# Optimization experiments

Hardware: AMD Instinct MI355X
Metric: run time of the kernel (lower is better)

## Reference

```python
import jax, jax.numpy as jnp
import numpy as np

T, B, D, H = 512, 256, 256, 256


def setup_inputs() -> dict:
    key = jax.random.key(0)
    ks = jax.random.split(key, 10)
    # ragged lengths in [T//2, T], sorted descending as pack_padded_sequence requires
    lengths = np.sort(np.random.RandomState(0).randint(T // 2, T + 1, size=B))[::-1]
    # batch_sizes[t] = number of sequences still active at step t (non-increasing, >=1)
    batch_sizes = (lengths[None, :] > np.arange(T)[:, None]).sum(axis=1).astype(np.int32)
    batch_sizes = np.maximum(batch_sizes, 1)
    return {
        "input_x": jax.random.normal(ks[0], (T, B, D), jnp.float32),
        "h0": jax.random.normal(ks[1], (B, H), jnp.float32),
        "c0": jax.random.normal(ks[2], (B, H), jnp.float32),
        # variational dropout masks (precomputed, applied multiplicatively every step)
        "mask_x": (jax.random.uniform(ks[3], (B, D)) > 0.3).astype(jnp.float32) / 0.7,
        "mask_h": (jax.random.uniform(ks[4], (B, H)) > 0.3).astype(jnp.float32) / 0.7,
        "W_ih": jax.random.normal(ks[5], (4 * H, D), jnp.float32) * 0.05,
        "W_hh": jax.random.normal(ks[6], (4 * H, H), jnp.float32) * 0.05,
        "b_ih": jax.random.normal(ks[7], (4 * H,), jnp.float32) * 0.05,
        "b_hh": jax.random.normal(ks[8], (4 * H,), jnp.float32) * 0.05,
        "batch_sizes": jnp.asarray(batch_sizes),
    }


def reference(input_x, h0, c0, mask_x, mask_h, W_ih, W_hh, b_ih, b_hh, batch_sizes):
    # Forward (is_reversed=False) variational-dropout LSTM over a packed sequence.
    # Packed data is kept padded [T,B,*]; batch_sizes gives active rows per step.
    # Inactive rows keep their last-active hidden/cell state (== hn semantics).
    Bsz, Hid = h0.shape
    row = jnp.arange(Bsz)[:, None]

    def step(carry, inp):
        h, c = carry
        x_t, size = inp
        active = row < size  # [B,1]
        xi = x_t * mask_x            # input variational dropout
        hi = h * mask_h              # hidden variational dropout
        gates = xi @ W_ih.T + b_ih + hi @ W_hh.T + b_hh  # [B, 4H]
        i, f, g, o = jnp.split(gates, 4, axis=-1)
        c_new = jax.nn.sigmoid(f) * c + jax.nn.sigmoid(i) * jnp.tanh(g)
        h_new = jax.nn.sigmoid(o) * jnp.tanh(c_new)
        h = jnp.where(active, h_new, h)
        c = jnp.where(active, c_new, c)
        out = jnp.where(active, h_new, 0.0)  # padded positions zeroed (unused in pack)
        return (h, c), out

    (hn, cn), output = jax.lax.scan(step, (h0, c0), (input_x, batch_sizes))
    return output, hn, cn
```

## Files before the change

### kernel.cpp

```cpp
#include <hip/hip_runtime.h>
#include <hip/hip_bf16.h>

#define T_STEPS 512
#define BATCH   256
#define DIM     256
#define HID     256

using bf16x8  = __attribute__((ext_vector_type(8))) __bf16;
using floatx4 = __attribute__((ext_vector_type(4))) float;

__device__ __forceinline__ float sigf(float x)   { return 1.0f / (1.0f + __expf(-x)); }
__device__ __forceinline__ float tanh_f(float x) { return 1.0f - 2.0f / (1.0f + __expf(2.0f * x)); }

__device__ __forceinline__ bf16x8 cvt8(const float* p) {
  floatx4 a = *(const floatx4*)p;
  floatx4 b = *(const floatx4*)(p + 4);
  bf16x8 r;
  r[0]=(__bf16)a[0]; r[1]=(__bf16)a[1]; r[2]=(__bf16)a[2]; r[3]=(__bf16)a[3];
  r[4]=(__bf16)b[0]; r[5]=(__bf16)b[1]; r[6]=(__bf16)b[2]; r[7]=(__bf16)b[3];
  return r;
}

__device__ __forceinline__ void stage16(__bf16* sbuf, int srow, int cb, const float* v) {
  bf16x8 lo, hi;
  #pragma unroll
  for (int e = 0; e < 8; ++e) { lo[e] = (__bf16)v[e]; hi[e] = (__bf16)v[8 + e]; }
  const int base = srow * 512 + cb * 2;
  const int swz  = (srow & 7) << 4;
  *(bf16x8*)((char*)sbuf + (base ^ swz))        = lo;
  *(bf16x8*)((char*)sbuf + ((base + 16) ^ swz)) = hi;
}

__global__ void init_ws(int* __restrict__ bar) { bar[threadIdx.x] = 0; }

__global__ __launch_bounds__(256, 1) void lstm_s8(
    const float* __restrict__ x, const float* __restrict__ h0,
    const float* __restrict__ c0,
    const float* __restrict__ mask_x, const float* __restrict__ mask_h,
    const float* __restrict__ W_ih, const float* __restrict__ W_hh,
    const float* __restrict__ b_ih, const float* __restrict__ b_hh,
    const int* __restrict__ bs_g,
    float* __restrict__ out, float* __restrict__ hn_out, float* __restrict__ cn_out,
    int* __restrict__ flg, float* __restrict__ mb) {

  const int tid = threadIdx.x;
  const int g   = blockIdx.x & 15;
  const int s   = blockIdx.x >> 4;
  const int row_base = g * 16;
  const int lane = tid & 63;
  const int w    = tid >> 6;
  const int l15  = lane & 15;
  const int l4   = lane >> 4;

  const int crow  = tid >> 4;
  const int cv    = tid & 15;
  const int gcol0 = s * 32 + cv;
  const int gcol1 = gcol0 + 16;

  const int srow = tid & 15;
  const int cb   = (tid >> 4) * 16;

  __shared__ alignas(16) __bf16 s_x[16 * 256];
  __shared__ alignas(16) __bf16 s_h[16 * 256];
  __shared__ alignas(16) float  s_gates[16 * 128];
  __shared__ int s_bs[T_STEPS];

  for (int i = tid; i < T_STEPS; i += 256) s_bs[i] = bs_g[i];

  bf16x8 wih[2][8], whh[2][8];
  #pragma unroll
  for (int Tt = 0; Tt < 2; ++Tt) {
    const size_t wr = (size_t)(w * 256 + s * 32 + Tt * 16 + l15) * 256;
    #pragma unroll
    for (int m = 0; m < 8; ++m) {
      wih[Tt][m] = cvt8(W_ih + wr + m * 32 + l4 * 8);
      whh[Tt][m] = cvt8(W_hh + wr + m * 32 + l4 * 8);
    }
  }

  floatx4 mxs[4], mhs[4];
  #pragma unroll
  for (int jj = 0; jj < 4; ++jj) {
    mxs[jj] = *(const floatx4*)(mask_x + (row_base + srow) * DIM + cb + jj * 4);
    mhs[jj] = *(const floatx4*)(mask_h + (row_base + srow) * HID + cb + jj * 4);
  }

  float bb[4][2];
  #pragma unroll
  for (int q = 0; q < 4; ++q) {
    bb[q][0] = b_ih[q * 256 + gcol0] + b_hh[q * 256 + gcol0];
    bb[q][1] = b_ih[q * 256 + gcol1] + b_hh[q * 256 + gcol1];
  }

  float c_[2], h_[2];
  c_[0] = c0[(row_base + crow) * HID + gcol0];
  c_[1] = c0[(row_base + crow) * HID + gcol1];
  h_[0] = h0[(row_base + crow) * HID + gcol0];
  h_[1] = h0[(row_base + crow) * HID + gcol1];

  {
    float v[16];
    #pragma unroll
    for (int jj = 0; jj < 4; ++jj) {
      floatx4 hv = *(const floatx4*)(h0 + (row_base + srow) * HID + cb + jj * 4);
      v[jj*4+0] = hv[0] * mhs[jj][0]; v[jj*4+1] = hv[1] * mhs[jj][1];
      v[jj*4+2] = hv[2] * mhs[jj][2]; v[jj*4+3] = hv[3] * mhs[jj][3];
    }
    stage16(s_h, srow, cb, v);
    #pragma unroll
    for (int jj = 0; jj < 4; ++jj) {
      floatx4 xv = *(const floatx4*)(x + (size_t)(row_base + srow) * DIM + cb + jj * 4);
      v[jj*4+0] = xv[0] * mxs[jj][0]; v[jj*4+1] = xv[1] * mxs[jj][1];
      v[jj*4+2] = xv[2] * mxs[jj][2]; v[jj*4+3] = xv[3] * mxs[jj][3];
    }
    stage16(s_x, srow, cb, v);
  }
  __syncthreads();

  const int aswz = (l15 & 7) << 4;
  const int ab0  = l15 * 512 + l4 * 16;

  for (int t = 0; t < T_STEPS; ++t) {
    const int bszt = s_bs[t];
    if (bszt <= row_base) {
      float* op = out + (size_t)t * (BATCH * HID) + (row_base + crow) * HID;
      op[gcol0] = 0.0f; op[gcol1] = 0.0f;
      continue;
    }
    const bool act_n = (t + 1 < T_STEPS) && (s_bs[t + 1] > row_base);

    floatx4 xpf[4];
    if (act_n) {
      const float* xp = x + ((size_t)(t + 1) * BATCH + row_base + srow) * DIM + cb;
      #pragma unroll
      for (int jj = 0; jj < 4; ++jj) xpf[jj] = *(const floatx4*)(xp + jj * 4);
    }

    floatx4 acc0, acc1;
    acc0 = acc1 = (floatx4)(0.0f);
    #pragma unroll
    for (int m = 0; m < 8; ++m) {
      const int ab = (ab0 + m * 64) ^ aswz;
      bf16x8 ax = *(const bf16x8*)((const char*)s_x + ab);
      bf16x8 ah = *(const bf16x8*)((const char*)s_h + ab);
      acc0 = __builtin_amdgcn_mfma_f32_16x16x32_bf16(ax, wih[0][m], acc0, 0, 0, 0);
      acc0 = __builtin_amdgcn_mfma_f32_16x16x32_bf16(ah, whh[0][m], acc0, 0, 0, 0);
      acc1 = __builtin_amdgcn_mfma_f32_16x16x32_bf16(ax, wih[1][m], acc1, 0, 0, 0);
      acc1 = __builtin_amdgcn_mfma_f32_16x16x32_bf16(ah, whh[1][m], acc1, 0, 0, 0);
    }
    #pragma unroll
    for (int e = 0; e < 4; ++e) {
      s_gates[(l4 * 4 + e) * 128 + w * 32 + l15]      = acc0[e];
      s_gates[(l4 * 4 + e) * 128 + w * 32 + 16 + l15] = acc1[e];
    }
    __syncthreads();

    {
      const bool ract = (row_base + crow) < bszt;
      float o0, o1;
      #pragma unroll
      for (int k = 0; k < 2; ++k) {
        const int cc2 = cv + k * 16;
        const float gi = s_gates[crow * 128 + 0 * 32 + cc2];
        const float gf = s_gates[crow * 128 + 1 * 32 + cc2];
        const float gg = s_gates[crow * 128 + 2 * 32 + cc2];
        const float go = s_gates[crow * 128 + 3 * 32 + cc2];
        const float iv = sigf(gi + bb[0][k]);
        const float fv = sigf(gf + bb[1][k]);
        const float gv = tanh_f(gg + bb[2][k]);
        const float ov = sigf(go + bb[3][k]);
        const float cc = fv * c_[k] + iv * gv;
        const float hh = ov * tanh_f(cc);
        if (ract) { c_[k] = cc; h_[k] = hh; }
        (k ? o1 : o0) = ract ? hh : 0.0f;
      }
      float* op = out + (size_t)t * (BATCH * HID) + (row_base + crow) * HID;
      op[gcol0] = o0; op[gcol1] = o1;
      if (act_n) {
        float* mbw = mb + ((t + 1) & 1) * (BATCH * HID) + (row_base + crow) * HID;
        __hip_atomic_store(mbw + gcol0, h_[0], __ATOMIC_RELAXED, __HIP_MEMORY_SCOPE_AGENT);
        __hip_atomic_store(mbw + gcol1, h_[1], __ATOMIC_RELAXED, __HIP_MEMORY_SCOPE_AGENT);
      }
    }

    if (act_n) {
      {
        float v[16];
        #pragma unroll
        for (int jj = 0; jj < 4; ++jj) {
          v[jj*4+0] = xpf[jj][0] * mxs[jj][0]; v[jj*4+1] = xpf[jj][1] * mxs[jj][1];
          v[jj*4+2] = xpf[jj][2] * mxs[jj][2]; v[jj*4+3] = xpf[jj][3] * mxs[jj][3];
        }
        stage16(s_x, srow, cb, v);
      }
      asm volatile("s_waitcnt vmcnt(0)" ::: "memory");
      __syncthreads();
      const int target = t + 1;
      if (tid == 0)
        __hip_atomic_store(flg + g * 8 + s, target, __ATOMIC_RELAXED, __HIP_MEMORY_SCOPE_AGENT);
      int fv_;
      do {
        fv_ = __hip_atomic_load(flg + g * 8 + (lane & 7), __ATOMIC_RELAXED, __HIP_MEMORY_SCOPE_AGENT);
      } while (!__all(fv_ >= target));
      asm volatile("" ::: "memory");

      {
        const float* mbr = mb + ((t + 1) & 1) * (BATCH * HID) + (row_base + srow) * HID + cb;
        float v[16];
        #pragma unroll
        for (int j = 0; j < 8; ++j) {
          union { unsigned long long u; float f[2]; } uu;
          uu.u = __hip_atomic_load((const unsigned long long*)(mbr + j * 2),
                                   __ATOMIC_RELAXED, __HIP_MEMORY_SCOPE_AGENT);
          v[j * 2]     = uu.f[0];
          v[j * 2 + 1] = uu.f[1];
        }
        #pragma unroll
        for (int jj = 0; jj < 4; ++jj) {
          v[jj*4+0] *= mhs[jj][0]; v[jj*4+1] *= mhs[jj][1];
          v[jj*4+2] *= mhs[jj][2]; v[jj*4+3] *= mhs[jj][3];
        }
        stage16(s_h, srow, cb, v);
      }
      __syncthreads();
    }
  }

  hn_out[(row_base + crow) * HID + gcol0] = h_[0];
  hn_out[(row_base + crow) * HID + gcol1] = h_[1];
  cn_out[(row_base + crow) * HID + gcol0] = c_[0];
  cn_out[(row_base + crow) * HID + gcol1] = c_[1];
}

extern "C" void kernel_launch(void* const* d_in, const int* in_sizes, int n_in,
                              void* d_out, int out_size, void* d_ws, size_t ws_size,
                              hipStream_t stream) {
  const float* x      = (const float*)d_in[0];
  const float* h0     = (const float*)d_in[1];
  const float* c0     = (const float*)d_in[2];
  const float* mask_x = (const float*)d_in[3];
  const float* mask_h = (const float*)d_in[4];
  const float* W_ih   = (const float*)d_in[5];
  const float* W_hh   = (const float*)d_in[6];
  const float* b_ih   = (const float*)d_in[7];
  const float* b_hh   = (const float*)d_in[8];
  const int*   bs     = (const int*)d_in[9];

  float* out = (float*)d_out;
  float* hn  = out + (size_t)T_STEPS * BATCH * HID;
  float* cn  = hn + (size_t)BATCH * HID;

  int*   flg = (int*)d_ws;
  float* mb  = (float*)((char*)d_ws + 1024);

  init_ws<<<1, 256, 0, stream>>>(flg);
  lstm_s8<<<128, 256, 0, stream>>>(x, h0, c0, mask_x, mask_h, W_ih, W_hh,
                                   b_ih, b_hh, bs, out, hn, cn, flg, mb);
}
```

Before: 1.598 ms.

## Split LSTM across 4 column slices with 512-thread blocks and overlap x-GEMM with barrier wait

Drops the per-group slice count from 8 to 4 (64 blocks of 512 threads, 8 waves each), so each cross-block barrier involves fewer participants. The input projection MFMAs for step t now run before spinning on the flag, which hides part of the inter-block wait, and only the hidden-state MFMAs follow the h exchange. Gate staging uses a padded, swizzled layout, and raw s_barrier replaces __syncthreads. In exchange each block does twice the work per step and holds more weight registers per wave.

After: 1.918 ms. 20.0% more time.

```diff
diff --git a/kernel.cpp b/kernel.cpp
--- a/kernel.cpp
+++ b/kernel.cpp
@@ -5,6 +5,8 @@
 #define BATCH   256
 #define DIM     256
 #define HID     256
+#define NGRP    16
+#define NS      4
 
 using bf16x8  = __attribute__((ext_vector_type(8))) __bf16;
 using floatx4 = __attribute__((ext_vector_type(4))) float;
@@ -21,19 +23,9 @@
   return r;
 }
 
-__device__ __forceinline__ void stage16(__bf16* sbuf, int srow, int cb, const float* v) {
-  bf16x8 lo, hi;
-  #pragma unroll
-  for (int e = 0; e < 8; ++e) { lo[e] = (__bf16)v[e]; hi[e] = (__bf16)v[8 + e]; }
-  const int base = srow * 512 + cb * 2;
-  const int swz  = (srow & 7) << 4;
-  *(bf16x8*)((char*)sbuf + (base ^ swz))        = lo;
-  *(bf16x8*)((char*)sbuf + ((base + 16) ^ swz)) = hi;
-}
-
 __global__ void init_ws(int* __restrict__ bar) { bar[threadIdx.x] = 0; }
 
-__global__ __launch_bounds__(256, 1) void lstm_s8(
+__global__ __launch_bounds__(512, 2) void lstm_s4(
     const float* __restrict__ x, const float* __restrict__ h0,
     const float* __restrict__ c0,
     const float* __restrict__ mask_x, const float* __restrict__ mask_h,
@@ -43,193 +35,216 @@
     float* __restrict__ out, float* __restrict__ hn_out, float* __restrict__ cn_out,
     int* __restrict__ flg, float* __restrict__ mb) {
 
-  const int tid = threadIdx.x;
-  const int g   = blockIdx.x & 15;
-  const int s   = blockIdx.x >> 4;
+  const int tid  = threadIdx.x;
+  const int g    = blockIdx.x & 15;
+  const int s    = blockIdx.x >> 4;
   const int row_base = g * 16;
   const int lane = tid & 63;
   const int w    = tid >> 6;
   const int l15  = lane & 15;
   const int l4   = lane >> 4;
 
-  const int crow  = tid >> 4;
-  const int cv    = tid & 15;
-  const int gcol0 = s * 32 + cv;
-  const int gcol1 = gcol0 + 16;
+  const int q  = w >> 1;
+  const int cB = s * 64 + (w & 1) * 32;
 
   const int srow = tid & 15;
-  const int cb   = (tid >> 4) * 16;
+  const int scb  = (tid >> 4) * 8;
+
+  const int crow  = tid >> 5;
+  const int colL0 = tid & 31;
 
   __shared__ alignas(16) __bf16 s_x[16 * 256];
   __shared__ alignas(16) __bf16 s_h[16 * 256];
-  __shared__ alignas(16) float  s_gates[16 * 128];
+  __shared__ float s_gates[256 * 17];
   __shared__ int s_bs[T_STEPS];
 
-  for (int i = tid; i < T_STEPS; i += 256) s_bs[i] = bs_g[i];
-
-  bf16x8 wih[2][8], whh[2][8];
+  for (int i = tid; i < T_STEPS; i += 512) s_bs[i] = bs_g[i];
+
+  bf16x8 wih_r[16], whh_r[16];
   #pragma unroll
-  for (int Tt = 0; Tt < 2; ++Tt) {
-    const size_t wr = (size_t)(w * 256 + s * 32 + Tt * 16 + l15) * 256;
+  for (int tt = 0; tt < 2; ++tt) {
+    const size_t wr = (size_t)(q * HID + cB + tt * 16 + l15) * DIM;
     #pragma unroll
     for (int m = 0; m < 8; ++m) {
-      wih[Tt][m] = cvt8(W_ih + wr + m * 32 + l4 * 8);
-      whh[Tt][m] = cvt8(W_hh + wr + m * 32 + l4 * 8);
-    }
-  }
-
-  floatx4 mxs[4], mhs[4];
+      wih_r[tt * 8 + m] = cvt8(W_ih + wr + m * 32 + l4 * 8);
+      whh_r[tt * 8 + m] = cvt8(W_hh + wr + m * 32 + l4 * 8);
+    }
+  }
+
+  floatx4 mxs[2], mhs[2];
+  mxs[0] = *(const floatx4*)(mask_x + (row_base + srow) * DIM + scb);
+  mxs[1] = *(const floatx4*)(mask_x + (row_base + srow) * DIM + scb + 4);
+  mhs[0] = *(const floatx4*)(mask_h + (row_base + srow) * HID + scb);
+  mhs[1] = *(const floatx4*)(mask_h + (row_base + srow) * HID + scb + 4);
+
+  float bb[4][2], c_[2], h_[2];
   #pragma unroll
-  for (int jj = 0; jj < 4; ++jj) {
-    mxs[jj] = *(const floatx4*)(mask_x + (row_base + srow) * DIM + cb + jj * 4);
-    mhs[jj] = *(const floatx4*)(mask_h + (row_base + srow) * HID + cb + jj * 4);
-  }
-
-  float bb[4][2];
-  #pragma unroll
-  for (int q = 0; q < 4; ++q) {
-    bb[q][0] = b_ih[q * 256 + gcol0] + b_hh[q * 256 + gcol0];
-    bb[q][1] = b_ih[q * 256 + gcol1] + b_hh[q * 256 + gcol1];
-  }
-
-  float c_[2], h_[2];
-  c_[0] = c0[(row_base + crow) * HID + gcol0];
-  c_[1] = c0[(row_base + crow) * HID + gcol1];
-  h_[0] = h0[(row_base + crow) * HID + gcol0];
-  h_[1] = h0[(row_base + crow) * HID + gcol1];
-
+  for (int qq = 0; qq < 4; ++qq) {
+    bb[qq][0] = b_ih[qq * HID + s * 64 + colL0]      + b_hh[qq * HID + s * 64 + colL0];
+    bb[qq][1] = b_ih[qq * HID + s * 64 + colL0 + 32] + b_hh[qq * HID + s * 64 + colL0 + 32];
+  }
+  c_[0] = c0[(row_base + crow) * HID + s * 64 + colL0];
+  c_[1] = c0[(row_base + crow) * HID + s * 64 + colL0 + 32];
+  h_[0] = h0[(row_base + crow) * HID + s * 64 + colL0];
+  h_[1] = h0[(row_base + crow) * HID + s * 64 + colL0 + 32];
+
+  const int soff = ((srow * 512 + scb * 2) ^ ((srow & 7) << 4));
   {
-    float v[16];
-    #pragma unroll
-    for (int jj = 0; jj < 4; ++jj) {
-      floatx4 hv = *(const floatx4*)(h0 + (row_base + srow) * HID + cb + jj * 4);
-      v[jj*4+0] = hv[0] * mhs[jj][0]; v[jj*4+1] = hv[1] * mhs[jj][1];
-      v[jj*4+2] = hv[2] * mhs[jj][2]; v[jj*4+3] = hv[3] * mhs[jj][3];
-    }
-    stage16(s_h, srow, cb, v);
-    #pragma unroll
-    for (int jj = 0; jj < 4; ++jj) {
-      floatx4 xv = *(const floatx4*)(x + (size_t)(row_base + srow) * DIM + cb + jj * 4);
-      v[jj*4+0] = xv[0] * mxs[jj][0]; v[jj*4+1] = xv[1] * mxs[jj][1];
-      v[jj*4+2] = xv[2] * mxs[jj][2]; v[jj*4+3] = xv[3] * mxs[jj][3];
-    }
-    stage16(s_x, srow, cb, v);
+    float v[8];
+    floatx4 h0a = *(const floatx4*)(h0 + (row_base + srow) * HID + scb);
+    floatx4 h0b = *(const floatx4*)(h0 + (row_base + srow) * HID + scb + 4);
+    #pragma unroll
+    for (int e = 0; e < 4; ++e) { v[e] = h0a[e] * mhs[0][e]; v[4+e] = h0b[e] * mhs[1][e]; }
+    bf16x8 hb;
+    #pragma unroll
+    for (int e = 0; e < 8; ++e) hb[e] = (__bf16)v[e];
+    *(bf16x8*)((char*)s_h + soff) = hb;
+
+    floatx4 x0a = *(const floatx4*)(x + (size_t)(row_base + srow) * DIM + scb);
+    floatx4 x0b = *(const floatx4*)(x + (size_t)(row_base + srow) * DIM + scb + 4);
+    #pragma unroll
+    for (int e = 0; e < 4; ++e) { v[e] = x0a[e] * mxs[0][e]; v[4+e] = x0b[e] * mxs[1][e]; }
+    bf16x8 xb;
+    #pragma unroll
+    for (int e = 0; e < 8; ++e) xb[e] = (__bf16)v[e];
+    *(bf16x8*)((char*)s_x + soff) = xb;
   }
   __syncthreads();
 
   const int aswz = (l15 & 7) << 4;
   const int ab0  = l15 * 512 + l4 * 16;
+
+  int* flgp = flg + g * 32;
 
   for (int t = 0; t < T_STEPS; ++t) {
     const int bszt = s_bs[t];
     if (bszt <= row_base) {
-      float* op = out + (size_t)t * (BATCH * HID) + (row_base + crow) * HID;
-      op[gcol0] = 0.0f; op[gcol1] = 0.0f;
+      float* op = out + (size_t)t * (BATCH * HID) + (row_base + crow) * HID + s * 64;
+      op[colL0] = 0.0f; op[colL0 + 32] = 0.0f;
       continue;
     }
     const bool act_n = (t + 1 < T_STEPS) && (s_bs[t + 1] > row_base);
 
-    floatx4 xpf[4];
+    floatx4 xpf0, xpf1;
     if (act_n) {
-      const float* xp = x + ((size_t)(t + 1) * BATCH + row_base + srow) * DIM + cb;
-      #pragma unroll
-      for (int jj = 0; jj < 4; ++jj) xpf[jj] = *(const floatx4*)(xp + jj * 4);
-    }
-
-    floatx4 acc0, acc1;
-    acc0 = acc1 = (floatx4)(0.0f);
+      const float* xp = x + ((size_t)(t + 1) * BATCH + row_base + srow) * DIM + scb;
+      xpf0 = *(const floatx4*)xp;
+      xpf1 = *(const floatx4*)(xp + 4);
+    }
+
+    floatx4 a0, a1;
+    a0 = a1 = (floatx4)(0.0f);
     #pragma unroll
     for (int m = 0; m < 8; ++m) {
       const int ab = (ab0 + m * 64) ^ aswz;
       bf16x8 ax = *(const bf16x8*)((const char*)s_x + ab);
+      a0 = __builtin_amdgcn_mfma_f32_16x16x32_bf16(ax, wih_r[m],     a0, 0, 0, 0);
+      a1 = __builtin_amdgcn_mfma_f32_16x16x32_bf16(ax, wih_r[8 + m], a1, 0, 0, 0);
+    }
+
+    if (t > 0) {
+      int fv;
+      do {
+        fv = __hip_atomic_load(flgp + (lane & 3), __ATOMIC_RELAXED, __HIP_MEMORY_SCOPE_AGENT);
+      } while (!__all(fv >= t));
+      asm volatile("" ::: "memory");
+
+      const float* mbr = mb + (size_t)(t & 1) * (BATCH * HID) + (row_base + srow) * HID + scb;
+      float v[8];
+      #pragma unroll
+      for (int jj = 0; jj < 4; ++jj) {
+        union { unsigned long long u; float f[2]; } uu;
+        uu.u = __hip_atomic_load((const unsigned long long*)(mbr + jj * 2),
+                                 __ATOMIC_RELAXED, __HIP_MEMORY_SCOPE_AGENT);
+        v[jj * 2]     = uu.f[0];
+        v[jj * 2 + 1] = uu.f[1];
+      }
+      #pragma unroll
+      for (int e = 0; e < 4; ++e) { v[e] *= mhs[0][e]; v[4 + e] *= mhs[1][e]; }
+      bf16x8 hb;
+      #pragma unroll
+      for (int e = 0; e < 8; ++e) hb[e] = (__bf16)v[e];
+      *(bf16x8*)((char*)s_h + soff) = hb;
+    }
+
+    asm volatile("s_waitcnt lgkmcnt(0)" ::: "memory");
+    __builtin_amdgcn_s_barrier();
+
+    #pragma unroll
+    for (int m = 0; m < 8; ++m) {
+      const int ab = (ab0 + m * 64) ^ aswz;
       bf16x8 ah = *(const bf16x8*)((const char*)s_h + ab);
-      acc0 = __builtin_amdgcn_mfma_f32_16x16x32_bf16(ax, wih[0][m], acc0, 0, 0, 0);
-      acc0 = __builtin_amdgcn_mfma_f32_16x16x32_bf16(ah, whh[0][m], acc0, 0, 0, 0);
-      acc1 = __builtin_amdgcn_mfma_f32_16x16x32_bf16(ax, wih[1][m], acc1, 0, 0, 0);
-      acc1 = __builtin_amdgcn_mfma_f32_16x16x32_bf16(ah, whh[1][m], acc1, 0, 0, 0);
-    }
-    #pragma unroll
-    for (int e = 0; e < 4; ++e) {
-      s_gates[(l4 * 4 + e) * 128 + w * 32 + l15]      = acc0[e];
-      s_gates[(l4 * 4 + e) * 128 + w * 32 + 16 + l15] = acc1[e];
-    }
-    __syncthreads();
-
+      a0 = __builtin_amdgcn_mfma_f32_16x16x32_bf16(ah, whh_r[m],     a0, 0, 0, 0);
+      a1 = __builtin_amdgcn_mfma_f32_16x16x32_bf16(ah, whh_r[8 + m], a1, 0, 0, 0);
+    }
+
+    #pragma unroll
+    for (int tt = 0; tt < 2; ++tt) {
+      const int gc = q * 64 + (w & 1) * 32 + tt * 16 + l15;
+      const int pb = gc * 17 + 4 * (l4 ^ (gc & 3));
+      const floatx4 av = tt ? a1 : a0;
+      #pragma unroll
+      for (int e = 0; e < 4; ++e) s_gates[pb + e] = av[e];
+    }
+
+    asm volatile("s_waitcnt lgkmcnt(0)" ::: "memory");
+    __builtin_amdgcn_s_barrier();
+
+    float o_[2];
     {
       const bool ract = (row_base + crow) < bszt;
-      float o0, o1;
       #pragma unroll
       for (int k = 0; k < 2; ++k) {
-        const int cc2 = cv + k * 16;
-        const float gi = s_gates[crow * 128 + 0 * 32 + cc2];
-        const float gf = s_gates[crow * 128 + 1 * 32 + cc2];
-        const float gg = s_gates[crow * 128 + 2 * 32 + cc2];
-        const float go = s_gates[crow * 128 + 3 * 32 + cc2];
-        const float iv = sigf(gi + bb[0][k]);
-        const float fv = sigf(gf + bb[1][k]);
-        const float gv = tanh_f(gg + bb[2][k]);
-        const float ov = sigf(go + bb[3][k]);
+        const int colL = colL0 + 32 * k;
+        float gq[4];
+        #pragma unroll
+        for (int qq = 0; qq < 4; ++qq) {
+          const int gc = qq * 64 + colL;
+          gq[qq] = s_gates[gc * 17 + 4 * ((crow >> 2) ^ (gc & 3)) + (crow & 3)];
+        }
+        const float iv = sigf(gq[0] + bb[0][k]);
+        const float fv = sigf(gq[1] + bb[1][k]);
+        const float gv = tanh_f(gq[2] + bb[2][k]);
+        const float ov = sigf(gq[3] + bb[3][k]);
         const float cc = fv * c_[k] + iv * gv;
         const float hh = ov * tanh_f(cc);
         if (ract) { c_[k] = cc; h_[k] = hh; }
-        (k ? o1 : o0) = ract ? hh : 0.0f;
+        o_[k] = ract ? hh : 0.0f;
       }
-      float* op = out + (size_t)t * (BATCH * HID) + (row_base + crow) * HID;
-      op[gcol0] = o0; op[gcol1] = o1;
-      if (act_n) {
-        float* mbw = mb + ((t + 1) & 1) * (BATCH * HID) + (row_base + crow) * HID;
-        __hip_atomic_store(mbw + gcol0, h_[0], __ATOMIC_RELAXED, __HIP_MEMORY_SCOPE_AGENT);
-        __hip_atomic_store(mbw + gcol1, h_[1], __ATOMIC_RELAXED, __HIP_MEMORY_SCOPE_AGENT);
-      }
     }
 
     if (act_n) {
-      {
-        float v[16];
-        #pragma unroll
-        for (int jj = 0; jj < 4; ++jj) {
-          v[jj*4+0] = xpf[jj][0] * mxs[jj][0]; v[jj*4+1] = xpf[jj][1] * mxs[jj][1];
-          v[jj*4+2] = xpf[jj][2] * mxs[jj][2]; v[jj*4+3] = xpf[jj][3] * mxs[jj][3];
-        }
-        stage16(s_x, srow, cb, v);
-      }
+      float* mbw = mb + (size_t)((t + 1) & 1) * (BATCH * HID) + (row_base + crow) * HID + s * 64;
+      __hip_atomic_store(mbw + colL0,      h_[0], __ATOMIC_RELAXED, __HIP_MEMORY_SCOPE_AGENT);
+      __hip_atomic_store(mbw + colL0 + 32, h_[1], __ATOMIC_RELAXED, __HIP_MEMORY_SCOPE_AGENT);
       asm volatile("s_waitcnt vmcnt(0)" ::: "memory");
-      __syncthreads();
-      const int target = t + 1;
+      __builtin_amdgcn_s_barrier();
       if (tid == 0)
-        __hip_atomic_store(flg + g * 8 + s, target, __ATOMIC_RELAXED, __HIP_MEMORY_SCOPE_AGENT);
-      int fv_;
-      do {
-        fv_ = __hip_atomic_load(flg + g * 8 + (lane & 7), __ATOMIC_RELAXED, __HIP_MEMORY_SCOPE_AGENT);
-      } while (!__all(fv_ >= target));
-      asm volatile("" ::: "memory");
-
-      {
-        const float* mbr = mb + ((t + 1) & 1) * (BATCH * HID) + (row_base + srow) * HID + cb;
-        float v[16];
-        #pragma unroll
-        for (int j = 0; j < 8; ++j) {
-          union { unsigned long long u; float f[2]; } uu;
-          uu.u = __hip_atomic_load((const unsigned long long*)(mbr + j * 2),
-                                   __ATOMIC_RELAXED, __HIP_MEMORY_SCOPE_AGENT);
-          v[j * 2]     = uu.f[0];
-          v[j * 2 + 1] = uu.f[1];
-        }
-        #pragma unroll
-        for (int jj = 0; jj < 4; ++jj) {
-          v[jj*4+0] *= mhs[jj][0]; v[jj*4+1] *= mhs[jj][1];
-          v[jj*4+2] *= mhs[jj][2]; v[jj*4+3] *= mhs[jj][3];
-        }
-        stage16(s_h, srow, cb, v);
-      }
-      __syncthreads();
-    }
-  }
-
-  hn_out[(row_base + crow) * HID + gcol0] = h_[0];
-  hn_out[(row_base + crow) * HID + gcol1] = h_[1];
-  cn_out[(row_base + crow) * HID + gcol0] = c_[0];
-  cn_out[(row_base + crow) * HID + gcol1] = c_[1];
+        __hip_atomic_store(flgp + s, t + 1, __ATOMIC_RELAXED, __HIP_MEMORY_SCOPE_AGENT);
+    }
+
+    {
+      float* op = out + (size_t)t * (BATCH * HID) + (row_base + crow) * HID + s * 64;
+      op[colL0] = o_[0]; op[colL0 + 32] = o_[1];
+    }
+
+    if (act_n) {
+      float v[8];
+      #pragma unroll
+      for (int e = 0; e < 4; ++e) { v[e] = xpf0[e] * mxs[0][e]; v[4 + e] = xpf1[e] * mxs[1][e]; }
+      bf16x8 xb;
+      #pragma unroll
+      for (int e = 0; e < 8; ++e) xb[e] = (__bf16)v[e];
+      *(bf16x8*)((char*)s_x + soff) = xb;
+      asm volatile("s_waitcnt lgkmcnt(0)" ::: "memory");
+      __builtin_amdgcn_s_barrier();
+    }
+  }
+
+  hn_out[(row_base + crow) * HID + s * 64 + colL0]      = h_[0];
+  hn_out[(row_base + crow) * HID + s * 64 + colL0 + 32] = h_[1];
+  cn_out[(row_base + crow) * HID + s * 64 + colL0]      = c_[0];
+  cn_out[(row_base + crow) * HID + s * 64 + colL0 + 32] = c_[1];
 }
 
 extern "C" void kernel_launch(void* const* d_in, const int* in_sizes, int n_in,
@@ -251,9 +266,9 @@
   float* cn  = hn + (size_t)BATCH * HID;
 
   int*   flg = (int*)d_ws;
-  float* mb  = (float*)((char*)d_ws + 1024);
-
-  init_ws<<<1, 256, 0, stream>>>(flg);
-  lstm_s8<<<128, 256, 0, stream>>>(x, h0, c0, mask_x, mask_h, W_ih, W_hh,
-                                   b_ih, b_hh, bs, out, hn, cn, flg, mb);
+  float* mb  = (float*)((char*)d_ws + 4096);
+
+  init_ws<<<1, 512, 0, stream>>>(flg);
+  lstm_s4<<<NGRP * NS, 512, 0, stream>>>(x, h0, c0, mask_x, mask_h, W_ih, W_hh,
+                                         b_ih, b_hh, bs, out, hn, cn, flg, mb);
 }
```
